# Kernel tuning notes

Measured on AMD Instinct MI355X. Metric: run time of the kernel, lower is better.

The kernel has to match this reference:

```python
import jax, jax.numpy as jnp
import numpy as np

B, N, D, H, L, F = 8192, 64, 128, 8, 3, 512
HD = D // H
RADIUS = 3.0
LN_EPS = 1e-5


def _ln(x, g, b):
    m = jnp.mean(x, axis=-1, keepdims=True)
    v = jnp.var(x, axis=-1, keepdims=True)
    return (x - m) / jnp.sqrt(v + LN_EPS) * g + b


def setup_inputs() -> dict:
    key = jax.random.key(0)
    ks = jax.random.split(key, 20)
    def nrm(k, shape, s=0.05):
        return jax.random.normal(k, shape, jnp.float32) * s
    return {
        'ego_context': nrm(ks[0], (B, D), 1.0),
        'ego_pos': nrm(ks[1], (B, 2), 1.0),
        'ego_vel': nrm(ks[2], (B, 2), 1.0),
        'neighbor_pos': nrm(ks[3], (B, N, 2), 1.5),
        'neighbor_vel': nrm(ks[4], (B, N, 2), 1.0),
        'neighbor_mask': jax.random.bernoulli(ks[5], 0.8, (B, N)),
        'np_W': nrm(ks[6], (6, D), 0.3), 'np_b': jnp.zeros((D,), jnp.float32),
        'np_ln_g': jnp.ones((D,), jnp.float32), 'np_ln_b': jnp.zeros((D,), jnp.float32),
        'ego_W': nrm(ks[7], (D, D)), 'ego_b': jnp.zeros((D,), jnp.float32),
        'ego_ln_g': jnp.ones((D,), jnp.float32), 'ego_ln_b': jnp.zeros((D,), jnp.float32),
        'n1_g': jnp.ones((L, D), jnp.float32), 'n1_b': jnp.zeros((L, D), jnp.float32),
        'nkv_g': jnp.ones((L, D), jnp.float32), 'nkv_b': jnp.zeros((L, D), jnp.float32),
        'n2_g': jnp.ones((L, D), jnp.float32), 'n2_b': jnp.zeros((L, D), jnp.float32),
        'Wq': nrm(ks[8], (L, D, D)), 'bq': jnp.zeros((L, D), jnp.float32),
        'Wk': nrm(ks[9], (L, D, D)), 'bk': jnp.zeros((L, D), jnp.float32),
        'Wv': nrm(ks[10], (L, D, D)), 'bv': jnp.zeros((L, D), jnp.float32),
        'Wo': nrm(ks[11], (L, D, D)), 'bo': jnp.zeros((L, D), jnp.float32),
        'W1': nrm(ks[12], (L, D, F)), 'b1': jnp.zeros((L, F), jnp.float32),
        'W2': nrm(ks[13], (L, F, D)), 'b2': jnp.zeros((L, D), jnp.float32),
        'out_W': nrm(ks[14], (D, D)), 'out_b': jnp.zeros((D,), jnp.float32),
        'out_ln_g': jnp.ones((D,), jnp.float32), 'out_ln_b': jnp.zeros((D,), jnp.float32),
    }


def reference(ego_context, ego_pos, ego_vel, neighbor_pos, neighbor_vel, neighbor_mask,
              np_W, np_b, np_ln_g, np_ln_b, ego_W, ego_b, ego_ln_g, ego_ln_b,
              n1_g, n1_b, nkv_g, nkv_b, n2_g, n2_b,
              Wq, bq, Wk, bk, Wv, bv, Wo, bo, W1, b1, W2, b2,
              out_W, out_b, out_ln_g, out_ln_b):
    # relative features (B, N, 6)
    rel_pos = neighbor_pos - ego_pos[:, None, :]
    rel_vel = neighbor_vel - ego_vel[:, None, :]
    dist = jnp.clip(jnp.linalg.norm(rel_pos, axis=-1, keepdims=True), 1e-6, None)
    bearing = jnp.arctan2(rel_pos[..., 1:2] + 1e-8, rel_pos[..., 0:1] + 1e-8)
    rel = jnp.concatenate([rel_pos, rel_vel, dist, bearing], axis=-1)

    # dynamic mask: radius gating + all-masked fixup (mimics key_padding_mask[all_masked,0]=False)
    valid = neighbor_mask & (jnp.linalg.norm(neighbor_pos - ego_pos[:, None, :], axis=-1) < RADIUS)
    all_invalid = ~jnp.any(valid, axis=-1)
    valid = valid | (all_invalid[:, None] & (jnp.arange(N) == 0)[None, :])

    # neighbor_proj: Linear(6,D) -> LN -> ReLU (dropout inactive at eval)
    nb = jax.nn.relu(_ln(rel @ np_W + np_b, np_ln_g, np_ln_b))  # (B, N, D)
    # ego_proj: Linear(D,D) -> LN; keep ego as (B, D) since query length is 1
    x = _ln(ego_context @ ego_W + ego_b, ego_ln_g, ego_ln_b)

    scale = 1.0 / jnp.sqrt(jnp.float32(HD))
    for i in range(L):
        q = _ln(x, n1_g[i], n1_b[i])          # (B, D)
        kv = _ln(nb, nkv_g[i], nkv_b[i])      # (B, N, D)
        Q = (q @ Wq[i] + bq[i]).reshape(B, H, HD)
        K = (kv @ Wk[i] + bk[i]).reshape(B, N, H, HD)
        V = (kv @ Wv[i] + bv[i]).reshape(B, N, H, HD)
        scores = jnp.einsum('bhd,bnhd->bhn', Q, K) * scale
        scores = jnp.where(valid[:, None, :], scores, -1e9)
        attn = jax.nn.softmax(scores, axis=-1)
        ctx = jnp.einsum('bhn,bnhd->bhd', attn, V).reshape(B, D)
        x = x + ctx @ Wo[i] + bo[i]
        y = _ln(x, n2_g[i], n2_b[i])
        x = x + jax.nn.gelu(y @ W1[i] + b1[i], approximate=False) @ W2[i] + b2[i]

    return _ln(x @ out_W + out_b, out_ln_g, out_ln_b)
```

## Files before the change

### kernel.cpp

```cpp
#include <hip/hip_runtime.h>
#include <stdint.h>

typedef unsigned int uint;
typedef unsigned short ushort;
typedef unsigned long long u64;

#define B_   8192
#define D_   128
#define N_   64
#define L_   3

typedef __attribute__((ext_vector_type(8))) short short8;
typedef __attribute__((ext_vector_type(4))) float f32x4;
union FragU { uint4 u; short8 h; };

__device__ __forceinline__ float bf2f(ushort u){ union{uint i; float f;} c; c.i=((uint)u)<<16; return c.f; }
__device__ __forceinline__ float bflo(uint u){ union{uint i; float f;} c; c.i=u<<16; return c.f; }
__device__ __forceinline__ float bfhi(uint u){ union{uint i; float f;} c; c.i=u&0xffff0000u; return c.f; }
__device__ __forceinline__ ushort f2bf(float f){ uint u=__float_as_uint(f); return (ushort)((u + 0x7fffu + ((u>>16)&1u))>>16); }
__device__ __forceinline__ uint pk2(float lo, float hi){ return (uint)f2bf(lo) | (((uint)f2bf(hi))<<16); }
__device__ __forceinline__ float wsum(float v){ for (int o=32;o;o>>=1) v += __shfl_xor(v,o); return v; }

__device__ ushort g_WqT[3*128*128];
__device__ ushort g_WkT[3*128*128];
__device__ ushort g_WvT[3*128*128];
__device__ ushort g_WoT[3*128*128];
__device__ ushort g_W1T[3*512*128];
__device__ ushort g_W2T[3*128*512];
__device__ ushort g_egoT[128*128];
__device__ ushort g_outT[128*128];
__device__ float  g_npRec[128*9];
__device__ ushort g_bqF[384];
__device__ ushort g_bkF[384];
__device__ ushort g_bvF[384];
__device__ ushort g_b1F[1536];
__device__ u64    g_msk[B_];

#define OFF_X   0
#define XSTR    520
#define OFF_XH  8320
#define XHSTR   272
#define OFF_Q   12672
#define QSTR    260
#define OFF_QK  16832
#define QKSTR   272
#define OFF_QB  21184
#define OFF_V   21248
#define OFF_NB  21504
#define NBSTR   272
#define OFF_NT  38912
#define NTSTR   144
#define OFF_AT  57344
#define ATSTR   144
#define OFF_U   59648
#define USTR    272
#define OFF_CXH 61824
#define OFF_H1  21504
#define LDS_SZ  62272

struct P {
  const float *ego, *epos, *evel, *npos, *nvel;
  const int   *mask;
  const float *npW, *npb, *npg, *npbb;
  const float *ego_b, *ego_g, *ego_bb;
  const float *bo, *b2, *out_b, *out_g, *out_bb;
  ushort *nbg;
  float *outp;
};

template<int MODE>
__global__ __launch_bounds__(256,4) void prep_all(P p,
    const float* Wq,const float* bq,const float* n1g,const float* n1b,
    const float* Wk,const float* bk,const float* nkg,const float* nkb,
    const float* Wv,const float* bv,
    const float* W1,const float* b1,const float* n2g,const float* n2b,
    const float* Wo,const float* W2,const float* egoW,const float* outW){
  __shared__ float red[2];
  __shared__ float s_npW[768], s_npP[384];
  __shared__ float s_valid[2][64];
  const int bid = blockIdx.x;
  const int tid = threadIdx.x;
  if (bid < 2688){
    int t = tid;
    const float *src,*g,*bb,*bias; ushort *dstW,*dstB; int N;
    if (bid<384){ int l=bid>>7, j=bid&127; src=Wq+l*16384+j; g=n1g+l*128; bb=n1b+l*128; bias=bq+l*128+j; dstW=g_WqT+l*16384+j*128; dstB=g_bqF+l*128+j; N=128; }
    else if (bid<768){ int q=bid-384; int l=q>>7, j=q&127; src=Wk+l*16384+j; g=nkg+l*128; bb=nkb+l*128; bias=bk+l*128+j; dstW=g_WkT+l*16384+j*128; dstB=g_bkF+l*128+j; N=128; }
    else if (bid<1152){ int q=bid-768; int l=q>>7, j=q&127; src=Wv+l*16384+j; g=nkg+l*128; bb=nkb+l*128; bias=bv+l*128+j; dstW=g_WvT+l*16384+j*128; dstB=g_bvF+l*128+j; N=128; }
    else { int q=bid-1152; int l=q/512, j=q%512; src=W1+l*65536+j; g=n2g+l*128; bb=n2b+l*128; bias=b1+l*512+j; dstW=g_W1T+l*65536+j*128; dstB=g_b1F+l*512+j; N=512; }
    if (t<128){
      float wv = src[t*N];
      dstW[t] = f2bf(g[t]*wv);
      float pv = wsum(bb[t]*wv);
      if ((t&63)==0) red[t>>6]=pv;
    }
    __syncthreads();
    if (t==0) *dstB = f2bf(red[0]+red[1]+bias[0]);
  } else if (bid < 3712){
    int pb = bid - 2688, t = tid;
    if (t<128){
      if (pb<384){ int l=pb>>7, j=pb&127; g_WoT[l*16384+j*128+t] = f2bf(Wo[l*16384+t*128+j]); }
      else if (pb<768){ int q=pb-384; int l=q>>7, j=q&127;
        for (int k=t;k<512;k+=128) g_W2T[l*65536+j*512+k] = f2bf(W2[l*65536+k*128+j]); }
      else if (pb<896){ int j=pb-768; g_egoT[j*128+t]=f2bf(egoW[t*128+j]); }
      else { int j=pb-896; g_outT[j*128+t]=f2bf(outW[t*128+j]); }
    }
  } else if (bid == 3712){
    int t = tid;
    if (t<128){
      for (int r=0;r<6;++r) g_npRec[t*9+r]=p.npW[r*128+t];
      g_npRec[t*9+6]=p.npb[t]; g_npRec[t*9+7]=p.npg[t]; g_npRec[t*9+8]=p.npbb[t];
    }
  } else {
    const int bq2 = bid - 3713;
    const int g = tid>>7, t = tid&127;
    const int b = bq2*2+g;
    for (int i=tid;i<768;i+=256) s_npW[i]=p.npW[i];
    if (tid<128){ s_npP[tid]=p.npb[tid]; s_npP[128+tid]=p.npg[tid]; s_npP[256+tid]=p.npbb[tid]; }
    __syncthreads();
    int nn=t>>1, jh=t&1;
    float2 pn = ((const float2*)p.npos)[b*N_+nn];
    float2 vn = ((const float2*)p.nvel)[b*N_+nn];
    float2 pe = ((const float2*)p.epos)[b];
    float2 ve = ((const float2*)p.evel)[b];
    float rx=pn.x-pe.x, ry=pn.y-pe.y, rvx=vn.x-ve.x, rvy=vn.y-ve.y;
    float nrm = sqrtf(rx*rx+ry*ry);
    float dist = fmaxf(nrm,1e-6f), bear = atan2f(ry+1e-8f, rx+1e-8f);
    bool vld = (p.mask[b*N_+nn]!=0) && (nrm<3.0f);
    if (jh==0) s_valid[g][nn] = vld?1.f:0.f;
    float z[64]; float sa=0.f, sb=0.f;
    #pragma unroll
    for (int jj=0;jj<64;++jj){
      int j = jh*64+jj;
      float v = s_npP[j] + rx*s_npW[j] + ry*s_npW[128+j] + rvx*s_npW[256+j]
                         + rvy*s_npW[384+j] + dist*s_npW[512+j] + bear*s_npW[640+j];
      z[jj]=v; sa+=v; sb+=v*v;
    }
    sa += __shfl_xor(sa,1); sb += __shfl_xor(sb,1);
    float m1 = sa*0.0078125f, r1 = rsqrtf(sb*0.0078125f - m1*m1 + 1e-5f);
    float ta=0.f, tb=0.f;
    #pragma unroll
    for (int jj=0;jj<64;++jj){
      int j = jh*64+jj;
      float a = (z[jj]-m1)*r1*s_npP[128+j] + s_npP[256+j];
      a = fmaxf(a,0.f);
      z[jj]=a; ta+=a; tb+=a*a;
    }
    ta += __shfl_xor(ta,1); tb += __shfl_xor(tb,1);
    float m2 = ta*0.0078125f, r2 = rsqrtf(tb*0.0078125f - m2*m2 + 1e-5f);
    uint4* dst4 = (uint4*)((char*)p.nbg + (size_t)b*16384 + (size_t)t*128);
    #pragma unroll
    for (int q8=0;q8<8;++q8){
      uint prs[4];
      #pragma unroll
      for (int qi=0;qi<4;++qi){
        int q = q8*4+qi;
        prs[qi] = pk2((z[2*q]-m2)*r2, (z[2*q+1]-m2)*r2);
      }
      uint4 ov; ov.x=prs[0]; ov.y=prs[1]; ov.z=prs[2]; ov.w=prs[3];
      dst4[q8] = ov;
    }
    __syncthreads();
    if (tid<2){
      u64 m=0;
      for (int n=0;n<64;++n) if (s_valid[tid][n]>0.5f) m |= (1ULL<<n);
      g_msk[bq2*2+tid] = m;
    }
  }
}

__device__ __forceinline__ void ln_to_xh(char* smem, int tid){
  int b = tid>>4, pp = tid&15;
  const char* xr = smem + OFF_X + b*XSTR + pp*32;
  float v[8];
  #pragma unroll
  for (int i=0;i<4;++i){ float2 t2 = *(const float2*)(xr + i*8); v[2*i]=t2.x; v[2*i+1]=t2.y; }
  float s1=0.f, s2=0.f;
  #pragma unroll
  for (int i=0;i<8;++i){ s1+=v[i]; s2+=v[i]*v[i]; }
  for (int o=1;o<16;o<<=1){ s1 += __shfl_xor(s1,o); s2 += __shfl_xor(s2,o); }
  float m = s1*0.0078125f, rs = rsqrtf(s2*0.0078125f - m*m + 1e-5f);
  uint4 o4;
  o4.x = pk2((v[0]-m)*rs,(v[1]-m)*rs); o4.y = pk2((v[2]-m)*rs,(v[3]-m)*rs);
  o4.z = pk2((v[4]-m)*rs,(v[5]-m)*rs); o4.w = pk2((v[6]-m)*rs,(v[7]-m)*rs);
  *(uint4*)(smem + OFF_XH + b*XHSTR + pp*16) = o4;
}

__device__ __forceinline__ void ln_affine_inplace(char* smem, int tid, const float* g, const float* bb){
  int b = tid>>4, pp = tid&15;
  char* xr = smem + OFF_X + b*XSTR + pp*32;
  float v[8];
  #pragma unroll
  for (int i=0;i<4;++i){ float2 t2 = *(const float2*)(xr + i*8); v[2*i]=t2.x; v[2*i+1]=t2.y; }
  float s1=0.f, s2=0.f;
  #pragma unroll
  for (int i=0;i<8;++i){ s1+=v[i]; s2+=v[i]*v[i]; }
  for (int o=1;o<16;o<<=1){ s1 += __shfl_xor(s1,o); s2 += __shfl_xor(s2,o); }
  float m = s1*0.0078125f, rs = rsqrtf(s2*0.0078125f - m*m + 1e-5f);
  #pragma unroll
  for (int i=0;i<8;++i) v[i] = (v[i]-m)*rs*g[pp*8+i] + bb[pp*8+i];
  #pragma unroll
  for (int i=0;i<4;++i){ float2 t2; t2.x=v[2*i]; t2.y=v[2*i+1]; *(float2*)(xr + i*8) = t2; }
}

__device__ __forceinline__ void cvt_x_to_xh(char* smem, int tid){
  int b = tid>>4, pp = tid&15;
  const char* xr = smem + OFF_X + b*XSTR + pp*32;
  float v[8];
  #pragma unroll
  for (int i=0;i<4;++i){ float2 t2 = *(const float2*)(xr + i*8); v[2*i]=t2.x; v[2*i+1]=t2.y; }
  uint4 o4;
  o4.x=pk2(v[0],v[1]); o4.y=pk2(v[2],v[3]); o4.z=pk2(v[4],v[5]); o4.w=pk2(v[6],v[7]);
  *(uint4*)(smem + OFF_XH + b*XHSTR + pp*16) = o4;
}

__global__ __launch_bounds__(256,2) void st_main6(P p){
  __shared__ __align__(16) char smem[LDS_SZ];
  const int tid = threadIdx.x;
  const int w = tid>>6, l64 = tid&63;
  const int cc = l64&15, qq = l64>>4;
  const int bB = blockIdx.x*16;

  for (int i=tid;i<1088;i+=256) ((uint*)(smem+OFF_QK))[i]=0u;
  if (tid<16) ((float*)(smem+OFF_QB))[tid]=0.f;
  for (int i=tid;i<288;i+=256) ((uint*)(smem+OFF_AT+8*ATSTR))[i]=0u;

  {
    int b_=tid>>4, pp=tid&15;
    const float* src = p.ego + (size_t)(bB+b_)*128 + pp*8;
    float4 v0 = *(const float4*)src, v1 = *(const float4*)(src+4);
    uint4 o4; o4.x=pk2(v0.x,v0.y); o4.y=pk2(v0.z,v0.w); o4.z=pk2(v1.x,v1.y); o4.w=pk2(v1.z,v1.w);
    *(uint4*)(smem + OFF_XH + b_*XHSTR + pp*16) = o4;
  }
  __syncthreads();
  {
    #pragma unroll
    for (int i=0;i<2;++i){
      int nt = w*2+i;
      f32x4 acc = {0.f,0.f,0.f,0.f};
      #pragma unroll
      for (int kt=0;kt<4;++kt){
        FragU a,bF;
        a.u = *(const uint4*)(smem + OFF_XH + cc*XHSTR + kt*64 + qq*16);
        bF.u = *(const uint4*)(g_egoT + (nt*16+cc)*128 + kt*32 + qq*8);
        acc = __builtin_amdgcn_mfma_f32_16x16x32_bf16(a.h, bF.h, acc, 0,0,0);
      }
      int col = nt*16+cc;
      float bv = p.ego_b[col];
      #pragma unroll
      for (int r=0;r<4;++r) *(float*)(smem+OFF_X+(qq*4+r)*XSTR+col*4) = acc[r]+bv;
    }
  }
  __syncthreads();
  ln_affine_inplace(smem, tid, p.ego_g, p.ego_bb);
  __syncthreads();

  for (int li=0; li<L_; ++li){
    ln_to_xh(smem, tid);
    __syncthreads();
    {
      const ushort* W = g_WqT + li*16384;
      #pragma unroll
      for (int i=0;i<2;++i){
        int nt = w*2+i;
        f32x4 acc = {0.f,0.f,0.f,0.f};
        #pragma unroll
        for (int kt=0;kt<4;++kt){
          FragU a,bF;
          a.u = *(const uint4*)(smem + OFF_XH + cc*XHSTR + kt*64 + qq*16);
          bF.u = *(const uint4*)(W + (nt*16+cc)*128 + kt*32 + qq*8);
          acc = __builtin_amdgcn_mfma_f32_16x16x32_bf16(a.h, bF.h, acc, 0,0,0);
        }
        int col = nt*16+cc;
        float bv = bf2f(g_bqF[li*128+col]);
        ushort* Qm = (ushort*)(smem+OFF_Q);
        #pragma unroll
        for (int r=0;r<4;++r) Qm[(qq*4+r)*130 + col] = f2bf(acc[r]+bv);
      }
    }
    __syncthreads();

    for (int bl=0; bl<16; ++bl){
      const int b = bB + bl;
      {
        int n = w*16 + (l64>>2), seg = l64&3;
        if (seg==0){
          u64 mv = g_msk[b];
          *(float*)(smem+OFF_V+n*4) = ((mv>>n)&1ULL) ? 1.f : 0.f;
        }
        const uint4* src = (const uint4*)(p.nbg + (size_t)b*8192 + n*128);
        ushort* T = (ushort*)(smem+OFF_NT);
        #pragma unroll
        for (int i=0;i<4;++i){
          int ci = seg + i*4;
          uint4 v = src[ci];
          *(uint4*)(smem + OFF_NB + n*NBSTR + ci*16) = v;
          int d0 = ci*8;
          T[(d0+0)*72+n]=(ushort)v.x; T[(d0+1)*72+n]=(ushort)(v.x>>16);
          T[(d0+2)*72+n]=(ushort)v.y; T[(d0+3)*72+n]=(ushort)(v.y>>16);
          T[(d0+4)*72+n]=(ushort)v.z; T[(d0+5)*72+n]=(ushort)(v.z>>16);
          T[(d0+6)*72+n]=(ushort)v.w; T[(d0+7)*72+n]=(ushort)(v.w>>16);
        }
      }
      {
        int h = (w<<1) + (l64>>5);
        int d4 = (l64&31)*4;
        const ushort* Wk = g_WkT + li*16384;
        float a0=0.f,a1=0.f,a2=0.f,a3=0.f, qb=0.f;
        #pragma unroll
        for (int j=0;j<16;++j){
          float qv = bf2f(*(const ushort*)(smem + OFF_Q + bl*QSTR + (h*16+j)*2));
          uint2 wv = *(const uint2*)(Wk + (h*16+j)*128 + d4);
          a0 += qv*bflo(wv.x); a1 += qv*bfhi(wv.x);
          a2 += qv*bflo(wv.y); a3 += qv*bfhi(wv.y);
          qb += qv * bf2f(g_bkF[li*128 + h*16 + j]);
        }
        uint2 o; o.x = pk2(a0,a1); o.y = pk2(a2,a3);
        *(uint2*)(smem + OFF_QK + h*QKSTR + d4*2) = o;
        if ((l64&31)==0) *(float*)(smem+OFF_QB + h*4) = qb;
      }
      __syncthreads();

      {
        FragU bfr[4];
        #pragma unroll
        for (int kt=0;kt<4;++kt) bfr[kt].u = *(const uint4*)(smem + OFF_QK + cc*QKSTR + kt*64 + qq*16);
        f32x4 c[4];
        #pragma unroll
        for (int mt=0;mt<4;++mt){
          f32x4 acc = {0.f,0.f,0.f,0.f};
          #pragma unroll
          for (int kt=0;kt<4;++kt){
            FragU a; a.u = *(const uint4*)(smem + OFF_NB + (mt*16+cc)*NBSTR + kt*64 + qq*16);
            acc = __builtin_amdgcn_mfma_f32_16x16x32_bf16(a.h, bfr[kt].h, acc, 0,0,0);
          }
          c[mt]=acc;
        }
        float qbv = *(const float*)(smem+OFF_QB+cc*4);
        float fl[16]; float anyv=0.f;
        #pragma unroll
        for (int mt=0;mt<4;++mt)
          #pragma unroll
          for (int r=0;r<4;++r){
            int n = mt*16 + qq*4 + r;
            float f = *(const float*)(smem+OFF_V+n*4);
            fl[mt*4+r]=f; anyv+=f;
          }
        bool none = (__ballot(anyv>0.5f)==0ULL);
        float sc[16];
        #pragma unroll
        for (int mt=0;mt<4;++mt)
          #pragma unroll
          for (int r=0;r<4;++r){
            int k = mt*4+r; int n = mt*16+qq*4+r;
            bool ok = (fl[k]>0.5f) || (none && n==0);
            sc[k] = ok ? 0.25f*(c[mt][r]+qbv) : -1e9f;
          }
        float mx=-3e38f;
        #pragma unroll
        for (int k=0;k<16;++k) mx=fmaxf(mx,sc[k]);
        mx = fmaxf(mx,__shfl_xor(mx,16)); mx = fmaxf(mx,__shfl_xor(mx,32));
        float ex[16]; float se=0.f;
        #pragma unroll
        for (int k=0;k<16;++k){ ex[k]=__expf(sc[k]-mx); se+=ex[k]; }
        se += __shfl_xor(se,16); se += __shfl_xor(se,32);
        float inv = 1.f/se;
        if (w==0 && cc<8){
          ushort* A = (ushort*)(smem+OFF_AT);
          #pragma unroll
          for (int mt=0;mt<4;++mt)
            #pragma unroll
            for (int r=0;r<4;++r) A[cc*72 + (mt*16+qq*4+r)] = f2bf(ex[mt*4+r]*inv);
        }
      }
      __syncthreads();

      {
        #pragma unroll
        for (int i=0;i<2;++i){
          int nt = w*2 + i;
          f32x4 acc={0.f,0.f,0.f,0.f};
          #pragma unroll
          for (int kt=0;kt<2;++kt){
            FragU a,bF;
            a.u = *(const uint4*)(smem + OFF_AT + cc*ATSTR + kt*64 + qq*16);
            bF.u = *(const uint4*)(smem + OFF_NT + (nt*16+cc)*NTSTR + kt*64 + qq*16);
            acc = __builtin_amdgcn_mfma_f32_16x16x32_bf16(a.h, bF.h, acc, 0,0,0);
          }
          if (qq<2){
            ushort* U = (ushort*)(smem+OFF_U);
            #pragma unroll
            for (int r=0;r<4;++r) U[(qq*4+r)*136 + nt*16+cc] = f2bf(acc[r]);
          }
        }
      }
      __syncthreads();

      {
        FragU afr[4];
        #pragma unroll
        for (int kt=0;kt<4;++kt)
          afr[kt].u = *(const uint4*)(smem + OFF_U + (cc&7)*USTR + kt*64 + qq*16);
        #pragma unroll
        for (int i=0;i<2;++i){
          int nt = w*2+i;
          f32x4 acc={0.f,0.f,0.f,0.f};
          #pragma unroll
          for (int kt=0;kt<4;++kt){
            FragU bF; bF.u = *(const uint4*)(g_WvT + li*16384 + (nt*16+cc)*128 + kt*32 + qq*8);
            acc = __builtin_amdgcn_mfma_f32_16x16x32_bf16(afr[kt].h, bF.h, acc, 0,0,0);
          }
          if (qq == (nt>>2)){
            int j = nt*16+cc;
            ((ushort*)(smem+OFF_CXH))[j] = f2bf(acc[nt&3] + bf2f(g_bvF[li*128+j]));
          }
        }
      }
      __syncthreads();

      {
        FragU afr[4];
        #pragma unroll
        for (int kt=0;kt<4;++kt)
          afr[kt].u = *(const uint4*)(smem + OFF_CXH + kt*64 + qq*16);
        #pragma unroll
        for (int i=0;i<2;++i){
          int nt = w*2+i;
          f32x4 acc={0.f,0.f,0.f,0.f};
          #pragma unroll
          for (int kt=0;kt<4;++kt){
            FragU bF; bF.u = *(const uint4*)(g_WoT + li*16384 + (nt*16+cc)*128 + kt*32 + qq*8);
            acc = __builtin_amdgcn_mfma_f32_16x16x32_bf16(afr[kt].h, bF.h, acc, 0,0,0);
          }
          if (qq==0){
            int j = nt*16+cc;
            *(float*)(smem + OFF_X + bl*XSTR + j*4) += acc[0] + p.bo[li*128+j];
          }
        }
      }
      __syncthreads();
    }

    ln_to_xh(smem, tid);
    __syncthreads();
    {
      FragU afr[4];
      #pragma unroll
      for (int kt=0;kt<4;++kt) afr[kt].u = *(const uint4*)(smem+OFF_XH + cc*XHSTR + kt*64 + qq*16);
      const ushort* W = g_W1T + li*65536;
      ushort* H = (ushort*)(smem+OFF_H1);
      #pragma unroll
      for (int i=0;i<8;++i){
        int nt = w*8+i;
        f32x4 acc={0.f,0.f,0.f,0.f};
        #pragma unroll
        for (int kt=0;kt<4;++kt){
          FragU bF; bF.u = *(const uint4*)(W + (nt*16+cc)*128 + kt*32 + qq*8);
          acc = __builtin_amdgcn_mfma_f32_16x16x32_bf16(afr[kt].h, bF.h, acc, 0,0,0);
        }
        int col = nt*16+cc;
        float bv = bf2f(g_b1F[li*512+col]);
        #pragma unroll
        for (int r=0;r<4;++r){
          float v = acc[r]+bv;
          v = 0.5f*v*(1.f+erff(v*0.70710678118654752f));
          H[(qq*4+r)*520 + col] = f2bf(v);
        }
      }
    }
    __syncthreads();
    {
      const ushort* W = g_W2T + li*65536;
      #pragma unroll
      for (int i=0;i<2;++i){
        int nt = w*2+i;
        f32x4 acc={0.f,0.f,0.f,0.f};
        #pragma unroll
        for (int kt=0;kt<16;++kt){
          FragU a,bF;
          a.u = *(const uint4*)(smem+OFF_H1 + cc*1040 + kt*64 + qq*16);
          bF.u = *(const uint4*)(W + (nt*16+cc)*512 + kt*32 + qq*8);
          acc = __builtin_amdgcn_mfma_f32_16x16x32_bf16(a.h, bF.h, acc, 0,0,0);
        }
        int col = nt*16+cc;
        float bv = p.b2[li*128+col];
        #pragma unroll
        for (int r=0;r<4;++r){
          float* xp = (float*)(smem+OFF_X+(qq*4+r)*XSTR+col*4);
          *xp += acc[r]+bv;
        }
      }
    }
    __syncthreads();
  }

  cvt_x_to_xh(smem, tid);
  __syncthreads();
  {
    #pragma unroll
    for (int i=0;i<2;++i){
      int nt = w*2+i;
      f32x4 acc = {0.f,0.f,0.f,0.f};
      #pragma unroll
      for (int kt=0;kt<4;++kt){
        FragU a,bF;
        a.u = *(const uint4*)(smem + OFF_XH + cc*XHSTR + kt*64 + qq*16);
        bF.u = *(const uint4*)(g_outT + (nt*16+cc)*128 + kt*32 + qq*8);
        acc = __builtin_amdgcn_mfma_f32_16x16x32_bf16(a.h, bF.h, acc, 0,0,0);
      }
      int col = nt*16+cc;
      float bv = p.out_b[col];
      #pragma unroll
      for (int r=0;r<4;++r) *(float*)(smem+OFF_X+(qq*4+r)*XSTR+col*4) = acc[r]+bv;
    }
  }
  __syncthreads();
  {
    int b_=tid>>4, pp=tid&15;
    const char* xr = smem + OFF_X + b_*XSTR + pp*32;
    float v[8];
    #pragma unroll
    for (int i=0;i<4;++i){ float2 t2 = *(const float2*)(xr + i*8); v[2*i]=t2.x; v[2*i+1]=t2.y; }
    float s1=0.f, s2=0.f;
    #pragma unroll
    for (int i=0;i<8;++i){ s1+=v[i]; s2+=v[i]*v[i]; }
    for (int o=1;o<16;o<<=1){ s1 += __shfl_xor(s1,o); s2 += __shfl_xor(s2,o); }
    float m = s1*0.0078125f, rs = rsqrtf(s2*0.0078125f - m*m + 1e-5f);
    float4 o0,o1;
    o0.x=(v[0]-m)*rs*p.out_g[pp*8+0]+p.out_bb[pp*8+0];
    o0.y=(v[1]-m)*rs*p.out_g[pp*8+1]+p.out_bb[pp*8+1];
    o0.z=(v[2]-m)*rs*p.out_g[pp*8+2]+p.out_bb[pp*8+2];
    o0.w=(v[3]-m)*rs*p.out_g[pp*8+3]+p.out_bb[pp*8+3];
    o1.x=(v[4]-m)*rs*p.out_g[pp*8+4]+p.out_bb[pp*8+4];
    o1.y=(v[5]-m)*rs*p.out_g[pp*8+5]+p.out_bb[pp*8+5];
    o1.z=(v[6]-m)*rs*p.out_g[pp*8+6]+p.out_bb[pp*8+6];
    o1.w=(v[7]-m)*rs*p.out_g[pp*8+7]+p.out_bb[pp*8+7];
    float* dst = p.outp + (size_t)(bB+b_)*128 + pp*8;
    *(float4*)dst = o0; *(float4*)(dst+4) = o1;
  }
}

__global__ __launch_bounds__(256,2) void st_main0(P p){
  __shared__ __align__(16) char smem[LDS_SZ];
  const int tid = threadIdx.x;
  const int w = tid>>6, l64 = tid&63;
  const int cc = l64&15, qq = l64>>4;
  const int bB = blockIdx.x*16;

  for (int i=tid;i<1088;i+=256) ((uint*)(smem+OFF_QK))[i]=0u;
  if (tid<16) ((float*)(smem+OFF_QB))[tid]=0.f;
  for (int i=tid;i<288;i+=256) ((uint*)(smem+OFF_AT+8*ATSTR))[i]=0u;

  {
    int b_=tid>>4, pp=tid&15;
    const float* src = p.ego + (size_t)(bB+b_)*128 + pp*8;
    float4 v0 = *(const float4*)src, v1 = *(const float4*)(src+4);
    uint4 o4; o4.x=pk2(v0.x,v0.y); o4.y=pk2(v0.z,v0.w); o4.z=pk2(v1.x,v1.y); o4.w=pk2(v1.z,v1.w);
    *(uint4*)(smem + OFF_XH + b_*XHSTR + pp*16) = o4;
  }
  __syncthreads();
  {
    #pragma unroll
    for (int i=0;i<2;++i){
      int nt = w*2+i;
      f32x4 acc = {0.f,0.f,0.f,0.f};
      #pragma unroll
      for (int kt=0;kt<4;++kt){
        FragU a,bF;
        a.u = *(const uint4*)(smem + OFF_XH + cc*XHSTR + kt*64 + qq*16);
        bF.u = *(const uint4*)(g_egoT + (nt*16+cc)*128 + kt*32 + qq*8);
        acc = __builtin_amdgcn_mfma_f32_16x16x32_bf16(a.h, bF.h, acc, 0,0,0);
      }
      int col = nt*16+cc;
      float bv = p.ego_b[col];
      #pragma unroll
      for (int r=0;r<4;++r) *(float*)(smem+OFF_X+(qq*4+r)*XSTR+col*4) = acc[r]+bv;
    }
  }
  __syncthreads();
  ln_affine_inplace(smem, tid, p.ego_g, p.ego_bb);
  __syncthreads();

  for (int li=0; li<L_; ++li){
    ln_to_xh(smem, tid);
    __syncthreads();
    {
      const ushort* W = g_WqT + li*16384;
      #pragma unroll
      for (int i=0;i<2;++i){
        int nt = w*2+i;
        f32x4 acc = {0.f,0.f,0.f,0.f};
        #pragma unroll
        for (int kt=0;kt<4;++kt){
          FragU a,bF;
          a.u = *(const uint4*)(smem + OFF_XH + cc*XHSTR + kt*64 + qq*16);
          bF.u = *(const uint4*)(W + (nt*16+cc)*128 + kt*32 + qq*8);
          acc = __builtin_amdgcn_mfma_f32_16x16x32_bf16(a.h, bF.h, acc, 0,0,0);
        }
        int col = nt*16+cc;
        float bv = bf2f(g_bqF[li*128+col]);
        ushort* Qm = (ushort*)(smem+OFF_Q);
        #pragma unroll
        for (int r=0;r<4;++r) Qm[(qq*4+r)*130 + col] = f2bf(acc[r]+bv);
      }
    }
    __syncthreads();

    for (int bl=0; bl<16; ++bl){
      const int b = bB + bl;
      {
        int n = w*16 + (l64>>2), jq = l64&3;
        float2 pn = ((const float2*)p.npos)[b*N_+n];
        float2 vn = ((const float2*)p.nvel)[b*N_+n];
        float2 pe = ((const float2*)p.epos)[b];
        float2 ve = ((const float2*)p.evel)[b];
        float rx=pn.x-pe.x, ry=pn.y-pe.y, rvx=vn.x-ve.x, rvy=vn.y-ve.y;
        float nrm = sqrtf(rx*rx+ry*ry);
        float dist = fmaxf(nrm,1e-6f), bear = atan2f(ry+1e-8f, rx+1e-8f);
        if (jq==0){
          bool vld = (p.mask[b*N_+n]!=0) && (nrm<3.0f);
          *(float*)(smem+OFF_V+n*4) = vld?1.f:0.f;
        }
        float z[32]; float sa=0.f, sb=0.f;
        #pragma unroll
        for (int jj=0;jj<32;++jj){
          const float* rec = g_npRec + (jq*32+jj)*9;
          float4 r0 = *(const float4*)rec;
          float4 r1 = *(const float4*)(rec+4);
          float v = r1.z + rx*r0.x + ry*r0.y + rvx*r0.z + rvy*r0.w + dist*r1.x + bear*r1.y;
          z[jj]=v; sa+=v; sb+=v*v;
        }
        sa += __shfl_xor(sa,1); sb += __shfl_xor(sb,1);
        sa += __shfl_xor(sa,2); sb += __shfl_xor(sb,2);
        float m1 = sa*0.0078125f, r1s = rsqrtf(sb*0.0078125f - m1*m1 + 1e-5f);
        float ta=0.f, tb=0.f;
        #pragma unroll
        for (int jj=0;jj<32;++jj){
          const float* rec = g_npRec + (jq*32+jj)*9;
          float a = (z[jj]-m1)*r1s*rec[7] + rec[8];
          a = fmaxf(a,0.f);
          z[jj]=a; ta+=a; tb+=a*a;
        }
        ta += __shfl_xor(ta,1); tb += __shfl_xor(tb,1);
        ta += __shfl_xor(ta,2); tb += __shfl_xor(tb,2);
        float m2 = ta*0.0078125f, r2s = rsqrtf(tb*0.0078125f - m2*m2 + 1e-5f);
        ushort* T = (ushort*)(smem+OFF_NT);
        #pragma unroll
        for (int q2=0;q2<16;++q2){
          uint pr = pk2((z[2*q2]-m2)*r2s, (z[2*q2+1]-m2)*r2s);
          *(uint*)(smem + OFF_NB + n*NBSTR + jq*64 + q2*4) = pr;
          int d = jq*32 + q2*2;
          T[d*72 + n] = (ushort)pr;
          T[(d+1)*72 + n] = (ushort)(pr>>16);
        }
      }
      {
        int h = (w<<1) + (l64>>5);
        int d4 = (l64&31)*4;
        const ushort* Wk = g_WkT + li*16384;
        float a0=0.f,a1=0.f,a2=0.f,a3=0.f, qb=0.f;
        #pragma unroll
        for (int j=0;j<16;++j){
          float qv = bf2f(*(const ushort*)(smem + OFF_Q + bl*QSTR + (h*16+j)*2));
          uint2 wv = *(const uint2*)(Wk + (h*16+j)*128 + d4);
          a0 += qv*bflo(wv.x); a1 += qv*bfhi(wv.x);
          a2 += qv*bflo(wv.y); a3 += qv*bfhi(wv.y);
          qb += qv * bf2f(g_bkF[li*128 + h*16 + j]);
        }
        uint2 o; o.x = pk2(a0,a1); o.y = pk2(a2,a3);
        *(uint2*)(smem + OFF_QK + h*QKSTR + d4*2) = o;
        if ((l64&31)==0) *(float*)(smem+OFF_QB + h*4) = qb;
      }
      __syncthreads();

      {
        FragU bfr[4];
        #pragma unroll
        for (int kt=0;kt<4;++kt) bfr[kt].u = *(const uint4*)(smem + OFF_QK + cc*QKSTR + kt*64 + qq*16);
        f32x4 c[4];
        #pragma unroll
        for (int mt=0;mt<4;++mt){
          f32x4 acc = {0.f,0.f,0.f,0.f};
          #pragma unroll
          for (int kt=0;kt<4;++kt){
            FragU a; a.u = *(const uint4*)(smem + OFF_NB + (mt*16+cc)*NBSTR + kt*64 + qq*16);
            acc = __builtin_amdgcn_mfma_f32_16x16x32_bf16(a.h, bfr[kt].h, acc, 0,0,0);
          }
          c[mt]=acc;
        }
        float qbv = *(const float*)(smem+OFF_QB+cc*4);
        float fl[16]; float anyv=0.f;
        #pragma unroll
        for (int mt=0;mt<4;++mt)
          #pragma unroll
          for (int r=0;r<4;++r){
            int n = mt*16 + qq*4 + r;
            float f = *(const float*)(smem+OFF_V+n*4);
            fl[mt*4+r]=f; anyv+=f;
          }
        bool none = (__ballot(anyv>0.5f)==0ULL);
        float sc[16];
        #pragma unroll
        for (int mt=0;mt<4;++mt)
          #pragma unroll
          for (int r=0;r<4;++r){
            int k = mt*4+r; int n = mt*16+qq*4+r;
            bool ok = (fl[k]>0.5f) || (none && n==0);
            sc[k] = ok ? 0.25f*(c[mt][r]+qbv) : -1e9f;
          }
        float mx=-3e38f;
        #pragma unroll
        for (int k=0;k<16;++k) mx=fmaxf(mx,sc[k]);
        mx = fmaxf(mx,__shfl_xor(mx,16)); mx = fmaxf(mx,__shfl_xor(mx,32));
        float ex[16]; float se=0.f;
        #pragma unroll
        for (int k=0;k<16;++k){ ex[k]=__expf(sc[k]-mx); se+=ex[k]; }
        se += __shfl_xor(se,16); se += __shfl_xor(se,32);
        float inv = 1.f/se;
        if (w==0 && cc<8){
          ushort* A = (ushort*)(smem+OFF_AT);
          #pragma unroll
          for (int mt=0;mt<4;++mt)
            #pragma unroll
            for (int r=0;r<4;++r) A[cc*72 + (mt*16+qq*4+r)] = f2bf(ex[mt*4+r]*inv);
        }
      }
      __syncthreads();

      {
        #pragma unroll
        for (int i=0;i<2;++i){
          int nt = w*2 + i;
          f32x4 acc={0.f,0.f,0.f,0.f};
          #pragma unroll
          for (int kt=0;kt<2;++kt){
            FragU a,bF;
            a.u = *(const uint4*)(smem + OFF_AT + cc*ATSTR + kt*64 + qq*16);
            bF.u = *(const uint4*)(smem + OFF_NT + (nt*16+cc)*NTSTR + kt*64 + qq*16);
            acc = __builtin_amdgcn_mfma_f32_16x16x32_bf16(a.h, bF.h, acc, 0,0,0);
          }
          if (qq<2){
            ushort* U = (ushort*)(smem+OFF_U);
            #pragma unroll
            for (int r=0;r<4;++r) U[(qq*4+r)*136 + nt*16+cc] = f2bf(acc[r]);
          }
        }
      }
      __syncthreads();

      {
        FragU afr[4];
        #pragma unroll
        for (int kt=0;kt<4;++kt)
          afr[kt].u = *(const uint4*)(smem + OFF_U + (cc&7)*USTR + kt*64 + qq*16);
        #pragma unroll
        for (int i=0;i<2;++i){
          int nt = w*2+i;
          f32x4 acc={0.f,0.f,0.f,0.f};
          #pragma unroll
          for (int kt=0;kt<4;++kt){
            FragU bF; bF.u = *(const uint4*)(g_WvT + li*16384 + (nt*16+cc)*128 + kt*32 + qq*8);
            acc = __builtin_amdgcn_mfma_f32_16x16x32_bf16(afr[kt].h, bF.h, acc, 0,0,0);
          }
          if (qq == (nt>>2)){
            int j = nt*16+cc;
            ((ushort*)(smem+OFF_CXH))[j] = f2bf(acc[nt&3] + bf2f(g_bvF[li*128+j]));
          }
        }
      }
      __syncthreads();

      {
        FragU afr[4];
        #pragma unroll
        for (int kt=0;kt<4;++kt)
          afr[kt].u = *(const uint4*)(smem + OFF_CXH + kt*64 + qq*16);
        #pragma unroll
        for (int i=0;i<2;++i){
          int nt = w*2+i;
          f32x4 acc={0.f,0.f,0.f,0.f};
          #pragma unroll
          for (int kt=0;kt<4;++kt){
            FragU bF; bF.u = *(const uint4*)(g_WoT + li*16384 + (nt*16+cc)*128 + kt*32 + qq*8);
            acc = __builtin_amdgcn_mfma_f32_16x16x32_bf16(afr[kt].h, bF.h, acc, 0,0,0);
          }
          if (qq==0){
            int j = nt*16+cc;
            *(float*)(smem + OFF_X + bl*XSTR + j*4) += acc[0] + p.bo[li*128+j];
          }
        }
      }
      __syncthreads();
    }

    ln_to_xh(smem, tid);
    __syncthreads();
    {
      FragU afr[4];
      #pragma unroll
      for (int kt=0;kt<4;++kt) afr[kt].u = *(const uint4*)(smem+OFF_XH + cc*XHSTR + kt*64 + qq*16);
      const ushort* W = g_W1T + li*65536;
      ushort* H = (ushort*)(smem+OFF_H1);
      #pragma unroll
      for (int i=0;i<8;++i){
        int nt = w*8+i;
        f32x4 acc={0.f,0.f,0.f,0.f};
        #pragma unroll
        for (int kt=0;kt<4;++kt){
          FragU bF; bF.u = *(const uint4*)(W + (nt*16+cc)*128 + kt*32 + qq*8);
          acc = __builtin_amdgcn_mfma_f32_16x16x32_bf16(afr[kt].h, bF.h, acc, 0,0,0);
        }
        int col = nt*16+cc;
        float bv = bf2f(g_b1F[li*512+col]);
        #pragma unroll
        for (int r=0;r<4;++r){
          float v = acc[r]+bv;
          v = 0.5f*v*(1.f+erff(v*0.70710678118654752f));
          H[(qq*4+r)*520 + col] = f2bf(v);
        }
      }
    }
    __syncthreads();
    {
      const ushort* W = g_W2T + li*65536;
      #pragma unroll
      for (int i=0;i<2;++i){
        int nt = w*2+i;
        f32x4 acc={0.f,0.f,0.f,0.f};
        #pragma unroll
        for (int kt=0;kt<16;++kt){
          FragU a,bF;
          a.u = *(const uint4*)(smem+OFF_H1 + cc*1040 + kt*64 + qq*16);
          bF.u = *(const uint4*)(W + (nt*16+cc)*512 + kt*32 + qq*8);
          acc = __builtin_amdgcn_mfma_f32_16x16x32_bf16(a.h, bF.h, acc, 0,0,0);
        }
        int col = nt*16+cc;
        float bv = p.b2[li*128+col];
        #pragma unroll
        for (int r=0;r<4;++r){
          float* xp = (float*)(smem+OFF_X+(qq*4+r)*XSTR+col*4);
          *xp += acc[r]+bv;
        }
      }
    }
    __syncthreads();
  }

  cvt_x_to_xh(smem, tid);
  __syncthreads();
  {
    #pragma unroll
    for (int i=0;i<2;++i){
      int nt = w*2+i;
      f32x4 acc = {0.f,0.f,0.f,0.f};
      #pragma unroll
      for (int kt=0;kt<4;++kt){
        FragU a,bF;
        a.u = *(const uint4*)(smem + OFF_XH + cc*XHSTR + kt*64 + qq*16);
        bF.u = *(const uint4*)(g_outT + (nt*16+cc)*128 + kt*32 + qq*8);
        acc = __builtin_amdgcn_mfma_f32_16x16x32_bf16(a.h, bF.h, acc, 0,0,0);
      }
      int col = nt*16+cc;
      float bv = p.out_b[col];
      #pragma unroll
      for (int r=0;r<4;++r) *(float*)(smem+OFF_X+(qq*4+r)*XSTR+col*4) = acc[r]+bv;
    }
  }
  __syncthreads();
  {
    int b_=tid>>4, pp=tid&15;
    const char* xr = smem + OFF_X + b_*XSTR + pp*32;
    float v[8];
    #pragma unroll
    for (int i=0;i<4;++i){ float2 t2 = *(const float2*)(xr + i*8); v[2*i]=t2.x; v[2*i+1]=t2.y; }
    float s1=0.f, s2=0.f;
    #pragma unroll
    for (int i=0;i<8;++i){ s1+=v[i]; s2+=v[i]*v[i]; }
    for (int o=1;o<16;o<<=1){ s1 += __shfl_xor(s1,o); s2 += __shfl_xor(s2,o); }
    float m = s1*0.0078125f, rs = rsqrtf(s2*0.0078125f - m*m + 1e-5f);
    float4 o0,o1;
    o0.x=(v[0]-m)*rs*p.out_g[pp*8+0]+p.out_bb[pp*8+0];
    o0.y=(v[1]-m)*rs*p.out_g[pp*8+1]+p.out_bb[pp*8+1];
    o0.z=(v[2]-m)*rs*p.out_g[pp*8+2]+p.out_bb[pp*8+2];
    o0.w=(v[3]-m)*rs*p.out_g[pp*8+3]+p.out_bb[pp*8+3];
    o1.x=(v[4]-m)*rs*p.out_g[pp*8+4]+p.out_bb[pp*8+4];
    o1.y=(v[5]-m)*rs*p.out_g[pp*8+5]+p.out_bb[pp*8+5];
    o1.z=(v[6]-m)*rs*p.out_g[pp*8+6]+p.out_bb[pp*8+6];
    o1.w=(v[7]-m)*rs*p.out_g[pp*8+7]+p.out_bb[pp*8+7];
    float* dst = p.outp + (size_t)(bB+b_)*128 + pp*8;
    *(float4*)dst = o0; *(float4*)(dst+4) = o1;
  }
}

extern "C" void kernel_launch(void* const* d_in, const int* in_sizes, int n_in,
                              void* d_out, int out_size, void* d_ws, size_t ws_size,
                              hipStream_t stream){
  (void)in_sizes; (void)n_in; (void)out_size;
  char* ws = (char*)d_ws;
  const size_t NEED1 = (size_t)B_*16384;

  P p;
  p.ego=(const float*)d_in[0]; p.epos=(const float*)d_in[1]; p.evel=(const float*)d_in[2];
  p.npos=(const float*)d_in[3]; p.nvel=(const float*)d_in[4]; p.mask=(const int*)d_in[5];
  p.npW=(const float*)d_in[6]; p.npb=(const float*)d_in[7]; p.npg=(const float*)d_in[8]; p.npbb=(const float*)d_in[9];
  p.ego_b=(const float*)d_in[11]; p.ego_g=(const float*)d_in[12]; p.ego_bb=(const float*)d_in[13];
  p.bo=(const float*)d_in[27]; p.b2=(const float*)d_in[31];
  p.out_b=(const float*)d_in[33]; p.out_g=(const float*)d_in[34]; p.out_bb=(const float*)d_in[35];
  p.nbg = (ushort*)ws;
  p.outp=(float*)d_out;

  #define PREP_ARGS p, \
      (const float*)d_in[20],(const float*)d_in[21],(const float*)d_in[14],(const float*)d_in[15], \
      (const float*)d_in[22],(const float*)d_in[23],(const float*)d_in[16],(const float*)d_in[17], \
      (const float*)d_in[24],(const float*)d_in[25], \
      (const float*)d_in[28],(const float*)d_in[29],(const float*)d_in[18],(const float*)d_in[19], \
      (const float*)d_in[26],(const float*)d_in[30],(const float*)d_in[10],(const float*)d_in[32]

  if (ws_size >= NEED1){
    prep_all<1><<<3713 + B_/2, 256, 0, stream>>>(PREP_ARGS);
    st_main6<<<B_/16,256,0,stream>>>(p);
  } else {
    prep_all<0><<<3713, 256, 0, stream>>>(PREP_ARGS);
    st_main0<<<B_/16,256,0,stream>>>(p);
  }
  #undef PREP_ARGS
}
```

Before: 606.6 us.

## Fuse neighbor projection into main kernel prologue and keep validity mask in LDS

```diff
diff --git a/kernel.cpp b/kernel.cpp
--- a/kernel.cpp
+++ b/kernel.cpp
@@ -29,12 +29,11 @@
 __device__ ushort g_W2T[3*128*512];
 __device__ ushort g_egoT[128*128];
 __device__ ushort g_outT[128*128];
-__device__ float  g_npRec[128*9];
+__device__ float  g_npRec[128*12];
 __device__ ushort g_bqF[384];
 __device__ ushort g_bkF[384];
 __device__ ushort g_bvF[384];
 __device__ ushort g_b1F[1536];
-__device__ u64    g_msk[B_];
 
 #define OFF_X   0
 #define XSTR    520
@@ -55,6 +54,7 @@
 #define OFF_U   59648
 #define USTR    272
 #define OFF_CXH 61824
+#define OFF_MSK 62080
 #define OFF_H1  21504
 #define LDS_SZ  62272
 
@@ -68,7 +68,6 @@
   float *outp;
 };
 
-template<int MODE>
 __global__ __launch_bounds__(256,4) void prep_all(P p,
     const float* Wq,const float* bq,const float* n1g,const float* n1b,
     const float* Wk,const float* bk,const float* nkg,const float* nkb,
@@ -76,8 +75,6 @@
     const float* W1,const float* b1,const float* n2g,const float* n2b,
     const float* Wo,const float* W2,const float* egoW,const float* outW){
   __shared__ float red[2];
-  __shared__ float s_npW[768], s_npP[384];
-  __shared__ float s_valid[2][64];
   const int bid = blockIdx.x;
   const int tid = threadIdx.x;
   if (bid < 2688){
@@ -104,66 +101,12 @@
       else if (pb<896){ int j=pb-768; g_egoT[j*128+t]=f2bf(egoW[t*128+j]); }
       else { int j=pb-896; g_outT[j*128+t]=f2bf(outW[t*128+j]); }
     }
-  } else if (bid == 3712){
+  } else {
     int t = tid;
     if (t<128){
-      for (int r=0;r<6;++r) g_npRec[t*9+r]=p.npW[r*128+t];
-      g_npRec[t*9+6]=p.npb[t]; g_npRec[t*9+7]=p.npg[t]; g_npRec[t*9+8]=p.npbb[t];
-    }
-  } else {
-    const int bq2 = bid - 3713;
-    const int g = tid>>7, t = tid&127;
-    const int b = bq2*2+g;
-    for (int i=tid;i<768;i+=256) s_npW[i]=p.npW[i];
-    if (tid<128){ s_npP[tid]=p.npb[tid]; s_npP[128+tid]=p.npg[tid]; s_npP[256+tid]=p.npbb[tid]; }
-    __syncthreads();
-    int nn=t>>1, jh=t&1;
-    float2 pn = ((const float2*)p.npos)[b*N_+nn];
-    float2 vn = ((const float2*)p.nvel)[b*N_+nn];
-    float2 pe = ((const float2*)p.epos)[b];
-    float2 ve = ((const float2*)p.evel)[b];
-    float rx=pn.x-pe.x, ry=pn.y-pe.y, rvx=vn.x-ve.x, rvy=vn.y-ve.y;
-    float nrm = sqrtf(rx*rx+ry*ry);
-    float dist = fmaxf(nrm,1e-6f), bear = atan2f(ry+1e-8f, rx+1e-8f);
-    bool vld = (p.mask[b*N_+nn]!=0) && (nrm<3.0f);
-    if (jh==0) s_valid[g][nn] = vld?1.f:0.f;
-    float z[64]; float sa=0.f, sb=0.f;
-    #pragma unroll
-    for (int jj=0;jj<64;++jj){
-      int j = jh*64+jj;
-      float v = s_npP[j] + rx*s_npW[j] + ry*s_npW[128+j] + rvx*s_npW[256+j]
-                         + rvy*s_npW[384+j] + dist*s_npW[512+j] + bear*s_npW[640+j];
-      z[jj]=v; sa+=v; sb+=v*v;
-    }
-    sa += __shfl_xor(sa,1); sb += __shfl_xor(sb,1);
-    float m1 = sa*0.0078125f, r1 = rsqrtf(sb*0.0078125f - m1*m1 + 1e-5f);
-    float ta=0.f, tb=0.f;
-    #pragma unroll
-    for (int jj=0;jj<64;++jj){
-      int j = jh*64+jj;
-      float a = (z[jj]-m1)*r1*s_npP[128+j] + s_npP[256+j];
-      a = fmaxf(a,0.f);
-      z[jj]=a; ta+=a; tb+=a*a;
-    }
-    ta += __shfl_xor(ta,1); tb += __shfl_xor(tb,1);
-    float m2 = ta*0.0078125f, r2 = rsqrtf(tb*0.0078125f - m2*m2 + 1e-5f);
-    uint4* dst4 = (uint4*)((char*)p.nbg + (size_t)b*16384 + (size_t)t*128);
-    #pragma unroll
-    for (int q8=0;q8<8;++q8){
-      uint prs[4];
-      #pragma unroll
-      for (int qi=0;qi<4;++qi){
-        int q = q8*4+qi;
-        prs[qi] = pk2((z[2*q]-m2)*r2, (z[2*q+1]-m2)*r2);
-      }
-      uint4 ov; ov.x=prs[0]; ov.y=prs[1]; ov.z=prs[2]; ov.w=prs[3];
-      dst4[q8] = ov;
-    }
-    __syncthreads();
-    if (tid<2){
-      u64 m=0;
-      for (int n=0;n<64;++n) if (s_valid[tid][n]>0.5f) m |= (1ULL<<n);
-      g_msk[bq2*2+tid] = m;
+      for (int r=0;r<6;++r) g_npRec[t*12+r]=p.npW[r*128+t];
+      g_npRec[t*12+6]=p.npb[t]; g_npRec[t*12+7]=p.npg[t]; g_npRec[t*12+8]=p.npbb[t];
+      g_npRec[t*12+9]=0.f; g_npRec[t*12+10]=0.f; g_npRec[t*12+11]=0.f;
     }
   }
 }
@@ -213,12 +156,76 @@
   *(uint4*)(smem + OFF_XH + b*XHSTR + pp*16) = o4;
 }
 
-__global__ __launch_bounds__(256,2) void st_main6(P p){
+__device__ __forceinline__ uint evenbits(u64 x){
+  x &= 0x5555555555555555ULL;
+  x = (x | (x>>1))  & 0x3333333333333333ULL;
+  x = (x | (x>>2))  & 0x0F0F0F0F0F0F0F0FULL;
+  x = (x | (x>>4))  & 0x00FF00FF00FF00FFULL;
+  x = (x | (x>>8))  & 0x0000FFFF0000FFFFULL;
+  x = (x | (x>>16)) & 0x00000000FFFFFFFFULL;
+  return (uint)x;
+}
+
+__global__ __launch_bounds__(256,2) void st_main7(P p){
   __shared__ __align__(16) char smem[LDS_SZ];
   const int tid = threadIdx.x;
   const int w = tid>>6, l64 = tid&63;
   const int cc = l64&15, qq = l64>>4;
   const int bB = blockIdx.x*16;
+
+  {
+    const int g = tid>>7, t = tid&127;
+    const int nn = t>>1, jh = t&1;
+    const int half = t>>6;
+    for (int pass=0; pass<8; ++pass){
+      const int bl = pass*2+g;
+      const int b = bB + bl;
+      float2 pn = ((const float2*)p.npos)[b*N_+nn];
+      float2 vn = ((const float2*)p.nvel)[b*N_+nn];
+      float2 pe = ((const float2*)p.epos)[b];
+      float2 ve = ((const float2*)p.evel)[b];
+      float rx=pn.x-pe.x, ry=pn.y-pe.y, rvx=vn.x-ve.x, rvy=vn.y-ve.y;
+      float nrm = sqrtf(rx*rx+ry*ry);
+      float dist = fmaxf(nrm,1e-6f), bear = atan2f(ry+1e-8f, rx+1e-8f);
+      bool vld = (p.mask[b*N_+nn]!=0) && (nrm<3.0f);
+      float z[64]; float sa=0.f, sb=0.f;
+      #pragma unroll
+      for (int jj=0;jj<64;++jj){
+        const float* rec = g_npRec + (jh*64+jj)*12;
+        float4 r0 = *(const float4*)rec;
+        float4 r1 = *(const float4*)(rec+4);
+        float v = r1.z + rx*r0.x + ry*r0.y + rvx*r0.z + rvy*r0.w + dist*r1.x + bear*r1.y;
+        z[jj]=v; sa+=v; sb+=v*v;
+      }
+      sa += __shfl_xor(sa,1); sb += __shfl_xor(sb,1);
+      float m1 = sa*0.0078125f, r1s = rsqrtf(sb*0.0078125f - m1*m1 + 1e-5f);
+      float ta=0.f, tb=0.f;
+      #pragma unroll
+      for (int jj=0;jj<64;++jj){
+        const float* rec = g_npRec + (jh*64+jj)*12;
+        float a = (z[jj]-m1)*r1s*rec[7] + rec[8];
+        a = fmaxf(a,0.f);
+        z[jj]=a; ta+=a; tb+=a*a;
+      }
+      ta += __shfl_xor(ta,1); tb += __shfl_xor(tb,1);
+      float m2 = ta*0.0078125f, r2s = rsqrtf(tb*0.0078125f - m2*m2 + 1e-5f);
+      uint4* dst4 = (uint4*)((char*)p.nbg + (size_t)b*16384 + (size_t)t*128);
+      #pragma unroll
+      for (int q8=0;q8<8;++q8){
+        uint prs[4];
+        #pragma unroll
+        for (int qi=0;qi<4;++qi){
+          int q = q8*4+qi;
+          prs[qi] = pk2((z[2*q]-m2)*r2s, (z[2*q+1]-m2)*r2s);
+        }
+        uint4 ov; ov.x=prs[0]; ov.y=prs[1]; ov.z=prs[2]; ov.w=prs[3];
+        dst4[q8] = ov;
+      }
+      uint m32 = evenbits(__ballot(vld));
+      if (l64==0) *(uint*)(smem + OFF_MSK + bl*8 + half*4) = m32;
+    }
+  }
+  __syncthreads();
 
   for (int i=tid;i<1088;i+=256) ((uint*)(smem+OFF_QK))[i]=0u;
   if (tid<16) ((float*)(smem+OFF_QB))[tid]=0.f;
@@ -281,18 +288,40 @@
 
     for (int bl=0; bl<16; ++bl){
       const int b = bB + bl;
-      {
-        int n = w*16 + (l64>>2), seg = l64&3;
+      const int n = w*16 + (l64>>2), seg = l64&3;
+      uint4 nv[4];
+      {
+        const uint4* src = (const uint4*)(p.nbg + (size_t)b*8192 + n*128);
+        #pragma unroll
+        for (int i=0;i<4;++i) nv[i] = src[seg + i*4];
         if (seg==0){
-          u64 mv = g_msk[b];
+          u64 mv = *(const u64*)(smem + OFF_MSK + bl*8);
           *(float*)(smem+OFF_V+n*4) = ((mv>>n)&1ULL) ? 1.f : 0.f;
         }
-        const uint4* src = (const uint4*)(p.nbg + (size_t)b*8192 + n*128);
+      }
+      {
+        int h = (w<<1) + (l64>>5);
+        int d4 = (l64&31)*4;
+        const ushort* Wk = g_WkT + li*16384;
+        float a0=0.f,a1=0.f,a2=0.f,a3=0.f, qb=0.f;
+        #pragma unroll
+        for (int j=0;j<16;++j){
+          float qv = bf2f(*(const ushort*)(smem + OFF_Q + bl*QSTR + (h*16+j)*2));
+          uint2 wv = *(const uint2*)(Wk + (h*16+j)*128 + d4);
+          a0 += qv*bflo(wv.x); a1 += qv*bfhi(wv.x);
+          a2 += qv*bflo(wv.y); a3 += qv*bfhi(wv.y);
+          qb += qv * bf2f(g_bkF[li*128 + h*16 + j]);
+        }
+        uint2 o; o.x = pk2(a0,a1); o.y = pk2(a2,a3);
+        *(uint2*)(smem + OFF_QK + h*QKSTR + d4*2) = o;
+        if ((l64&31)==0) *(float*)(smem+OFF_QB + h*4) = qb;
+      }
+      {
         ushort* T = (ushort*)(smem+OFF_NT);
         #pragma unroll
         for (int i=0;i<4;++i){
           int ci = seg + i*4;
-          uint4 v = src[ci];
+          uint4 v = nv[i];
           *(uint4*)(smem + OFF_NB + n*NBSTR + ci*16) = v;
           int d0 = ci*8;
           T[(d0+0)*72+n]=(ushort)v.x; T[(d0+1)*72+n]=(ushort)(v.x>>16);
@@ -301,23 +330,6 @@
           T[(d0+6)*72+n]=(ushort)v.w; T[(d0+7)*72+n]=(ushort)(v.w>>16);
         }
       }
-      {
-        int h = (w<<1) + (l64>>5);
-        int d4 = (l64&31)*4;
-        const ushort* Wk = g_WkT + li*16384;
-        float a0=0.f,a1=0.f,a2=0.f,a3=0.f, qb=0.f;
-        #pragma unroll
-        for (int j=0;j<16;++j){
-          float qv = bf2f(*(const ushort*)(smem + OFF_Q + bl*QSTR + (h*16+j)*2));
-          uint2 wv = *(const uint2*)(Wk + (h*16+j)*128 + d4);
-          a0 += qv*bflo(wv.x); a1 += qv*bfhi(wv.x);
-          a2 += qv*bflo(wv.y); a3 += qv*bfhi(wv.y);
-          qb += qv * bf2f(g_bkF[li*128 + h*16 + j]);
-        }
-        uint2 o; o.x = pk2(a0,a1); o.y = pk2(a2,a3);
-        *(uint2*)(smem + OFF_QK + h*QKSTR + d4*2) = o;
-        if ((l64&31)==0) *(float*)(smem+OFF_QB + h*4) = qb;
-      }
       __syncthreads();
 
       {
@@ -341,8 +353,8 @@
         for (int mt=0;mt<4;++mt)
           #pragma unroll
           for (int r=0;r<4;++r){
-            int n = mt*16 + qq*4 + r;
-            float f = *(const float*)(smem+OFF_V+n*4);
+            int nb_ = mt*16 + qq*4 + r;
+            float f = *(const float*)(smem+OFF_V+nb_*4);
             fl[mt*4+r]=f; anyv+=f;
           }
         bool none = (__ballot(anyv>0.5f)==0ULL);
@@ -351,8 +363,8 @@
         for (int mt=0;mt<4;++mt)
           #pragma unroll
           for (int r=0;r<4;++r){
-            int k = mt*4+r; int n = mt*16+qq*4+r;
-            bool ok = (fl[k]>0.5f) || (none && n==0);
+            int k = mt*4+r; int nb_ = mt*16+qq*4+r;
+            bool ok = (fl[k]>0.5f) || (none && nb_==0);
             sc[k] = ok ? 0.25f*(c[mt][r]+qbv) : -1e9f;
           }
         float mx=-3e38f;
@@ -623,7 +635,7 @@
         float z[32]; float sa=0.f, sb=0.f;
         #pragma unroll
         for (int jj=0;jj<32;++jj){
-          const float* rec = g_npRec + (jq*32+jj)*9;
+          const float* rec = g_npRec + (jq*32+jj)*12;
           float4 r0 = *(const float4*)rec;
           float4 r1 = *(const float4*)(rec+4);
           float v = r1.z + rx*r0.x + ry*r0.y + rvx*r0.z + rvy*r0.w + dist*r1.x + bear*r1.y;
@@ -635,7 +647,7 @@
         float ta=0.f, tb=0.f;
         #pragma unroll
         for (int jj=0;jj<32;++jj){
-          const float* rec = g_npRec + (jq*32+jj)*9;
+          const float* rec = g_npRec + (jq*32+jj)*12;
           float a = (z[jj]-m1)*r1s*rec[7] + rec[8];
           a = fmaxf(a,0.f);
           z[jj]=a; ta+=a; tb+=a*a;
@@ -908,19 +920,16 @@
   p.nbg = (ushort*)ws;
   p.outp=(float*)d_out;
 
-  #define PREP_ARGS p, \
-      (const float*)d_in[20],(const float*)d_in[21],(const float*)d_in[14],(const float*)d_in[15], \
-      (const float*)d_in[22],(const float*)d_in[23],(const float*)d_in[16],(const float*)d_in[17], \
-      (const float*)d_in[24],(const float*)d_in[25], \
-      (const float*)d_in[28],(const float*)d_in[29],(const float*)d_in[18],(const float*)d_in[19], \
-      (const float*)d_in[26],(const float*)d_in[30],(const float*)d_in[10],(const float*)d_in[32]
+  prep_all<<<3713, 256, 0, stream>>>(p,
+      (const float*)d_in[20],(const float*)d_in[21],(const float*)d_in[14],(const float*)d_in[15],
+      (const float*)d_in[22],(const float*)d_in[23],(const float*)d_in[16],(const float*)d_in[17],
+      (const float*)d_in[24],(const float*)d_in[25],
+      (const float*)d_in[28],(const float*)d_in[29],(const float*)d_in[18],(const float*)d_in[19],
+      (const float*)d_in[26],(const float*)d_in[30],(const float*)d_in[10],(const float*)d_in[32]);
 
   if (ws_size >= NEED1){
-    prep_all<1><<<3713 + B_/2, 256, 0, stream>>>(PREP_ARGS);
-    st_main6<<<B_/16,256,0,stream>>>(p);
+    st_main7<<<B_/16,256,0,stream>>>(p);
   } else {
-    prep_all<0><<<3713, 256, 0, stream>>>(PREP_ARGS);
     st_main0<<<B_/16,256,0,stream>>>(p);
   }
-  #undef PREP_ARGS
 }
```

Measured after the change: 770.0 us. +26.9%, slower.
